# Kernel tuning notes

Measured on AMD Instinct MI355X. Metric: run time of the kernel, lower is better.

Reference implementation:

```python
import math
import jax, jax.numpy as jnp
import numpy as np

N_HEAD = 32
LAYER_NUMBER = 10  # cancels out: beta*alibi*L + alpha*QK^T*L = alibi + QK^T/sqrt(d)


def build_alibi(seq_len, n_head, dtype):
    # Faithful port of BLOOM's build_alibi_tensor -> [n_head, 1, seq_len]
    cp2 = 2 ** math.floor(math.log2(n_head))
    base = 2.0 ** (-(2.0 ** -(math.log2(cp2) - 3)))
    slopes = base ** np.arange(1, 1 + cp2)
    if cp2 != n_head:
        extra_base = 2.0 ** (-(2.0 ** -(math.log2(2 * cp2) - 3)))
        num_rem = min(cp2, n_head - cp2)
        slopes = np.concatenate([slopes, extra_base ** np.arange(1, 1 + 2 * num_rem, 2)])
    alibi = slopes[:, None, None] * np.arange(seq_len)[None, None, :]
    return jnp.asarray(alibi, dtype)


def setup_inputs() -> dict:
    key = jax.random.key(0)
    ks = jax.random.split(key, 6)
    B, S, H = 4, 1024, 4096
    return {
        "hidden_states": jax.random.normal(ks[0], (B, S, H), jnp.float32),
        "residual": jax.random.normal(ks[1], (B, S, H), jnp.float32),
        "qkv_w": jax.random.normal(ks[2], (3 * H, H), jnp.float32) * 0.02,
        "qkv_b": jnp.zeros((3 * H,), jnp.float32),
        "dense_w": jax.random.normal(ks[3], (H, H), jnp.float32) * 0.02,
        "dense_b": jnp.zeros((H,), jnp.float32),
    }


def reference(hidden_states, residual, qkv_w, qkv_b, dense_w, dense_b):
    B, S, H = hidden_states.shape
    nh = N_HEAD
    d = H // nh
    # fused qkv projection: [B,S,3H] -> [B,S,nh,3d] -> split
    mixed = (hidden_states @ qkv_w.T + qkv_b).reshape(B, S, nh, 3 * d)
    q, k, v = jnp.split(mixed, 3, axis=-1)  # each [B,S,nh,d]

    alibi = build_alibi(S, nh, hidden_states.dtype)  # [nh,1,S]
    # beta*alibi + alpha*QK^T, then *layer_number in scaled softmax == alibi + QK^T/sqrt(d)
    scores = jnp.einsum("bqhd,bkhd->bhqk", q, k) / math.sqrt(d) + alibi[None]  # [B,nh,S,S]

    causal = jnp.tril(jnp.ones((S, S), bool))  # [S,S], True = attend
    scores = jnp.where(causal, scores, jnp.asarray(-10000.0, scores.dtype))
    # softmax in fp32 (attention_softmax_in_fp32), then zero masked entries like *(~padded_causal_mask)
    probs = jax.nn.softmax(scores.astype(jnp.float32), axis=-1) * causal
    probs = probs.astype(v.dtype)

    ctx = jnp.einsum("bhqk,bkhd->bqhd", probs, v).reshape(B, S, H)
    out = ctx @ dense_w.T + dense_b + residual  # dropout_add with p=0 / eval
    return out
```

## Files before the change

kernel.cpp:

```cpp
#include <hip/hip_runtime.h>
#include <hip/hip_bf16.h>

typedef __attribute__((ext_vector_type(8))) short bf16x8;
typedef __attribute__((ext_vector_type(4))) short short4v;
typedef __attribute__((ext_vector_type(4))) float f32x4;

#define MFMA16(A, B, C) __builtin_amdgcn_mfma_f32_16x16x32_bf16((A), (B), (C), 0, 0, 0)
#define GLDS16(g, l)                                                            \
  __builtin_amdgcn_global_load_lds(                                             \
      (const __attribute__((address_space(1))) void*)(g),                       \
      (__attribute__((address_space(3))) void*)(l), 16, 0, 0)

__device__ __forceinline__ short f2bf(float f) {
  union { float f; unsigned u; } v; v.f = f;
  return (short)((v.u + 0x7fffu + ((v.u >> 16) & 1u)) >> 16);
}

__device__ __forceinline__ void blk_barrier() {
  asm volatile("" ::: "memory");
  __builtin_amdgcn_s_barrier();
  asm volatile("" ::: "memory");
}

__global__ __launch_bounds__(256) void cvt_kernel(const float* __restrict__ in,
                                                  short* __restrict__ out, int n4) {
  int i = blockIdx.x * 256 + threadIdx.x;
  const int stride = gridDim.x * 256;
  for (; i < n4; i += stride) {
    f32x4 v = ((const f32x4*)in)[i];
    short4v o;
    o[0] = f2bf(v[0]); o[1] = f2bf(v[1]); o[2] = f2bf(v[2]); o[3] = f2bf(v[3]);
    ((short4v*)out)[i] = o;
  }
}

__global__ __launch_bounds__(512, 2) void gemm_bt8(const short* __restrict__ A,
                                                   const short* __restrict__ B,
                                                   const float* __restrict__ bias,
                                                   const float* __restrict__ resid,
                                                   short* __restrict__ Cb,
                                                   float* __restrict__ Cf,
                                                   int Mtiles, int Nn, int K, int mode) {
  __shared__ short sA[2][2][8192];
  __shared__ short sB[2][2][8192];
  const int tid = threadIdx.x;
  const int w = tid >> 6, l = tid & 63;
  const int wm = w >> 2, wn = w & 3;
  const int fr = l & 15, g4 = l >> 4, sx = l & 7;

  const int nwg = gridDim.x;
  const int qq = nwg >> 3, rr = nwg & 7;
  const int xcd = blockIdx.x & 7, sub = blockIdx.x >> 3;
  const int swz = (xcd < rr ? xcd * (qq + 1) : rr * (qq + 1) + (xcd - rr) * qq) + sub;
  const int rowBase = (swz % Mtiles) * 256;
  const int colBase = (swz / Mtiles) * 256;

  const int NT = K >> 6;
  const int swcol = ((l & 7) ^ (l >> 3)) * 8;
  const short* Ag = A + (size_t)(rowBase + w * 8 + (l >> 3)) * K + swcol;
  const short* Bg = B + (size_t)(colBase + w * 8 + (l >> 3)) * K + swcol;
  const size_t q1 = (size_t)64 * K;
  const size_t hh = (size_t)128 * K;

#define STAGE_A(buf, h, ko)                                     \
  GLDS16(Ag + (h) * hh + (ko), &sA[buf][h][w * 512]);           \
  GLDS16(Ag + (h) * hh + q1 + (ko), &sA[buf][h][(8 + w) * 512]);
#define STAGE_B(buf, h, ko)                                     \
  GLDS16(Bg + (h) * hh + (ko), &sB[buf][h][w * 512]);           \
  GLDS16(Bg + (h) * hh + q1 + (ko), &sB[buf][h][(8 + w) * 512]);
#define RD_A(buf, m, ks) \
  (*(const bf16x8*)&sA[buf][wm][(((m) * 16 + fr) << 6) + ((((ks) * 4 + g4) ^ sx) << 3)])
#define RD_B(buf, nf, ks) \
  (*(const bf16x8*)&sB[buf][wn >> 1][((((wn & 1) * 64) + (nf) * 16 + fr) << 6) + ((((ks) * 4 + g4) ^ sx) << 3)])

  f32x4 acc[8][4];
#pragma unroll
  for (int m = 0; m < 8; m++)
#pragma unroll
    for (int n = 0; n < 4; n++) acc[m][n] = (f32x4)(0.0f);

  STAGE_A(0, 0, 0); STAGE_A(0, 1, 0);
  STAGE_B(0, 0, 0); STAGE_B(0, 1, 0);

  for (int t = 0; t < NT; ++t) {
    const int cur = t & 1, nxt = cur ^ 1;
    const size_t ko = (size_t)(t + 1) << 6;
    bf16x8 bfr[4][2], af[2][2];
    if (t + 1 < NT) {
      STAGE_A(nxt, 0, ko); STAGE_A(nxt, 1, ko);
      asm volatile("s_waitcnt vmcnt(4)" ::: "memory");
    } else {
      asm volatile("s_waitcnt vmcnt(0)" ::: "memory");
    }
    blk_barrier();
#pragma unroll
    for (int nf = 0; nf < 4; nf++) {
      bfr[nf][0] = RD_B(cur, nf, 0);
      bfr[nf][1] = RD_B(cur, nf, 1);
    }
    af[0][0] = RD_A(cur, 0, 0); af[0][1] = RD_A(cur, 0, 1);
    af[1][0] = RD_A(cur, 1, 0); af[1][1] = RD_A(cur, 1, 1);
    __builtin_amdgcn_s_setprio(1);
#pragma unroll
    for (int mi = 0; mi < 2; mi++)
#pragma unroll
      for (int nf = 0; nf < 4; nf++) {
        acc[mi][nf] = MFMA16(af[mi][0], bfr[nf][0], acc[mi][nf]);
        acc[mi][nf] = MFMA16(af[mi][1], bfr[nf][1], acc[mi][nf]);
      }
    __builtin_amdgcn_s_setprio(0);
    blk_barrier();
#pragma unroll
    for (int p = 1; p < 4; p++) {
      af[0][0] = RD_A(cur, 2 * p, 0);     af[0][1] = RD_A(cur, 2 * p, 1);
      af[1][0] = RD_A(cur, 2 * p + 1, 0); af[1][1] = RD_A(cur, 2 * p + 1, 1);
      if (p == 1 && t + 1 < NT) {
        STAGE_B(nxt, 0, ko); STAGE_B(nxt, 1, ko);
      }
      blk_barrier();
      __builtin_amdgcn_s_setprio(1);
#pragma unroll
      for (int mi = 0; mi < 2; mi++)
#pragma unroll
        for (int nf = 0; nf < 4; nf++) {
          acc[2 * p + mi][nf] = MFMA16(af[mi][0], bfr[nf][0], acc[2 * p + mi][nf]);
          acc[2 * p + mi][nf] = MFMA16(af[mi][1], bfr[nf][1], acc[2 * p + mi][nf]);
        }
      __builtin_amdgcn_s_setprio(0);
      blk_barrier();
    }
  }

#pragma unroll
  for (int m = 0; m < 8; m++) {
    const int row0 = rowBase + wm * 128 + m * 16 + g4 * 4;
#pragma unroll
    for (int n = 0; n < 4; n++) {
      const int col = colBase + wn * 64 + n * 16 + fr;
      const float bc = bias[col];
#pragma unroll
      for (int j = 0; j < 4; j++) {
        const size_t idx = (size_t)(row0 + j) * Nn + col;
        const float v = acc[m][n][j] + bc;
        if (mode == 0) Cb[idx] = f2bf(v);
        else Cf[idx] = v + resid[idx];
      }
    }
  }
#undef STAGE_A
#undef STAGE_B
#undef RD_A
#undef RD_B
}

__global__ __launch_bounds__(256) void vtrans_kernel(const short* __restrict__ mixed,
                                                     short* __restrict__ vt) {
  __shared__ short tl[64][132];
  const int tid = threadIdx.x;
  const int st = blockIdx.x;
  const int bh = blockIdx.y;
  const int b = bh >> 5, h = bh & 31;
  const short* src = mixed + (size_t)(b * 1024 + st * 64) * 12288 + h * 384 + 256;
#pragma unroll
  for (int it = 0; it < 8; it++) {
    int idx = (tid + it * 256) * 4;
    int row = idx >> 7, col = idx & 127;
    *(short4v*)&tl[row][col] = *(const short4v*)(src + row * 12288 + col);
  }
  __syncthreads();
  short* dst = vt + (size_t)bh * 128 * 1024 + st * 64;
#pragma unroll
  for (int it = 0; it < 8; it++) {
    int o = (tid + it * 256) * 4;
    int d = o >> 6, t4 = o & 63;
    short4v w;
    w[0] = tl[t4][d]; w[1] = tl[t4 + 1][d]; w[2] = tl[t4 + 2][d]; w[3] = tl[t4 + 3][d];
    *(short4v*)(dst + d * 1024 + t4) = w;
  }
}

__global__ __launch_bounds__(256, 2) void attn_kernel(const short* __restrict__ mixed,
                                                      const short* __restrict__ vt,
                                                      short* __restrict__ ctx) {
  __shared__ short sK[2][64 * 128];
  __shared__ short sV[2][128 * 64];
  __shared__ unsigned p_lds[4][16 * 36];
  const int tid = threadIdx.x;
  const int w = tid >> 6, l = tid & 63;
  const int g = l >> 4, f = l & 15, f7 = l & 7;

  const int bidx = blockIdx.x;
  const int xcd = bidx & 7, idx = bidx >> 3;
  const int bh = (xcd << 4) | (idx >> 4);
  const int qt = idx & 15;
  const int b = bh >> 5, h = bh & 31;
  const int qw = qt * 64 + w * 16;
  const float scale = 0.08838834764831845f;
  const float slope = exp2f(-0.25f * (float)(h + 1));

  const short* qptr = mixed + (size_t)b * 1024 * 12288 + h * 384;
  const short* kptr = qptr + 128;
  const short* vtp = vt + (size_t)bh * 128 * 1024;

  bf16x8 qf[4];
  {
    const short* qrow = qptr + (size_t)(qw + f) * 12288 + (g << 3);
#pragma unroll
    for (int ks = 0; ks < 4; ks++) qf[ks] = *(const bf16x8*)(qrow + ks * 32);
  }

#define STAGE_K(buf, kt)                                                        \
  {                                                                             \
    _Pragma("unroll") for (int c4 = 0; c4 < 4; c4++) {                          \
      const int c = c4 * 4 + w;                                                 \
      const int r = c * 4 + (l >> 4);                                           \
      GLDS16(kptr + (size_t)((kt) + r) * 12288 + (((l & 15) ^ (r & 7)) << 3),   \
             &sK[buf][c << 9]);                                                 \
    }                                                                           \
  }
#define STAGE_V(buf, kt)                                                        \
  {                                                                             \
    _Pragma("unroll") for (int c4 = 0; c4 < 4; c4++) {                          \
      const int c = c4 * 4 + w;                                                 \
      const int r = c * 8 + (l >> 3);                                           \
      GLDS16(vtp + (size_t)r * 1024 + (kt) + (((l & 7) ^ (r & 7)) << 3),        \
             &sV[buf][c << 9]);                                                 \
    }                                                                           \
  }

  f32x4 acc[8];
#pragma unroll
  for (int n = 0; n < 8; n++) acc[n] = (f32x4)(0.0f);
  float mrun = -1e30f, lrun = 0.0f;
  const int q = qw + f;
  unsigned* pw = p_lds[w];

  const int TT = qt + 1;
  STAGE_K(0, 0);
  STAGE_V(0, 0);

  for (int t = 0; t < TT; ++t) {
    const int cur = t & 1, nxt = cur ^ 1;
    const int kt = t << 6;
    if (t + 1 < TT) {
      STAGE_K(nxt, kt + 64);
      STAGE_V(nxt, kt + 64);
      asm volatile("s_waitcnt vmcnt(8)" ::: "memory");
    } else {
      asm volatile("s_waitcnt vmcnt(0)" ::: "memory");
    }
    blk_barrier();

    f32x4 s[4];
#pragma unroll
    for (int ksub = 0; ksub < 4; ksub++) {
      s[ksub] = (f32x4)(0.0f);
      const int r = ksub * 16 + f;
#pragma unroll
      for (int ks = 0; ks < 4; ks++) {
        bf16x8 kf = *(const bf16x8*)&sK[cur][(r << 7) + ((((ks << 2) + g) ^ f7) << 3)];
        s[ksub] = MFMA16(kf, qf[ks], s[ksub]);
      }
    }

    float ev[4][4];
    float tmax = -1e30f;
#pragma unroll
    for (int ksub = 0; ksub < 4; ksub++)
#pragma unroll
      for (int j = 0; j < 4; j++) {
        const int k = kt + ksub * 16 + g * 4 + j;
        float v = s[ksub][j] * scale + slope * (float)k;
        if (k > q) v = -1e30f;
        ev[ksub][j] = v;
        tmax = fmaxf(tmax, v);
      }
    tmax = fmaxf(tmax, __shfl_xor(tmax, 16));
    tmax = fmaxf(tmax, __shfl_xor(tmax, 32));
    const float mnew = fmaxf(mrun, tmax);
    const float asc = __expf(mrun - mnew);
    float psum = 0.0f;
    unsigned* pr = pw + f * 36;
#pragma unroll
    for (int ksub = 0; ksub < 4; ksub++) {
      float e0 = __expf(ev[ksub][0] - mnew);
      float e1 = __expf(ev[ksub][1] - mnew);
      float e2 = __expf(ev[ksub][2] - mnew);
      float e3 = __expf(ev[ksub][3] - mnew);
      psum += (e0 + e1) + (e2 + e3);
      unsigned w0 = (unsigned)(unsigned short)f2bf(e0) |
                    ((unsigned)(unsigned short)f2bf(e1) << 16);
      unsigned w1 = (unsigned)(unsigned short)f2bf(e2) |
                    ((unsigned)(unsigned short)f2bf(e3) << 16);
      pr[ksub * 8 + g * 2] = w0;
      pr[ksub * 8 + g * 2 + 1] = w1;
    }
    psum += __shfl_xor(psum, 16);
    psum += __shfl_xor(psum, 32);
    lrun = lrun * asc + psum;
    mrun = mnew;

    float ascB[4];
#pragma unroll
    for (int j = 0; j < 4; j++) ascB[j] = __shfl(asc, 20 * g + j);
#pragma unroll
    for (int n = 0; n < 8; n++)
#pragma unroll
      for (int j = 0; j < 4; j++) acc[n][j] *= ascB[j];

    bf16x8 pa0 = *(const bf16x8*)(pw + f * 36 + (g << 2));
    bf16x8 pa1 = *(const bf16x8*)(pw + f * 36 + 16 + (g << 2));
#pragma unroll
    for (int n = 0; n < 8; n++) {
      const int dr = (n << 4) + f;
      bf16x8 vf0 = *(const bf16x8*)&sV[cur][(dr << 6) + ((g ^ f7) << 3)];
      acc[n] = MFMA16(pa0, vf0, acc[n]);
      bf16x8 vf1 = *(const bf16x8*)&sV[cur][(dr << 6) + (((4 + g) ^ f7) << 3)];
      acc[n] = MFMA16(pa1, vf1, acc[n]);
    }
    blk_barrier();
  }

  const float linv = 1.0f / lrun;
  float invB[4];
#pragma unroll
  for (int j = 0; j < 4; j++) invB[j] = __shfl(linv, 20 * g + j);
  const int trow = b * 1024 + qw + (g << 2);
#pragma unroll
  for (int n = 0; n < 8; n++) {
    const int col = h * 128 + (n << 4) + f;
#pragma unroll
    for (int j = 0; j < 4; j++)
      ctx[(size_t)(trow + j) * 4096 + col] = f2bf(acc[n][j] * invB[j]);
  }
#undef STAGE_K
#undef STAGE_V
}

extern "C" void kernel_launch(void* const* d_in, const int* in_sizes, int n_in,
                              void* d_out, int out_size, void* d_ws, size_t ws_size,
                              hipStream_t stream) {
  const float* hs = (const float*)d_in[0];
  const float* resid = (const float*)d_in[1];
  const float* qkv_w = (const float*)d_in[2];
  const float* qkv_b = (const float*)d_in[3];
  const float* dense_w = (const float*)d_in[4];
  const float* dense_b = (const float*)d_in[5];
  float* out = (float*)d_out;

  short* hs_b = (short*)d_ws;
  short* wqkv_b = hs_b + (size_t)16777216;
  short* wd_b = wqkv_b + (size_t)50331648;
  short* mixed = wd_b + (size_t)16777216;
  short* vt = wqkv_b;
  short* ctx = hs_b;

  cvt_kernel<<<1024, 256, 0, stream>>>(hs, hs_b, 16777216 / 4);
  cvt_kernel<<<1024, 256, 0, stream>>>(qkv_w, wqkv_b, 50331648 / 4);
  cvt_kernel<<<1024, 256, 0, stream>>>(dense_w, wd_b, 16777216 / 4);
  gemm_bt8<<<dim3(48 * 16), 512, 0, stream>>>(hs_b, wqkv_b, qkv_b, nullptr,
                                              mixed, nullptr, 16, 12288, 4096, 0);
  vtrans_kernel<<<dim3(16, 128), 256, 0, stream>>>(mixed, vt);
  attn_kernel<<<2048, 256, 0, stream>>>(mixed, vt, ctx);
  gemm_bt8<<<dim3(16 * 16), 512, 0, stream>>>(ctx, wd_b, dense_b, resid,
                                              nullptr, out, 16, 4096, 4096, 1);
}
```

Before: 808.3 us.

## Use smaller-tile double-buffered GEMM for dense projection to fill more CUs

Adds a new bf16 GEMM kernel with 128x256 tiles, K-step 32, double-buffered LDS via global_load_lds, an XCD-aware block swizzle and launch bounds allowing four blocks per CU. The dense output projection now uses it with 512 workgroups instead of 256 large-tile ones. The goal is to better occupy the 256 CUs on a GEMM that otherwise launches only one wave of blocks. The cost is shallower pipelining and more barriers per K step, since each step covers only 32 elements of K.

```diff
diff --git a/kernel.cpp b/kernel.cpp
--- a/kernel.cpp
+++ b/kernel.cpp
@@ -153,6 +153,92 @@
 #undef RD_B
 }
 
+__global__ __launch_bounds__(512, 4) void gemm_bt(const short* __restrict__ A,
+                                                  const short* __restrict__ B,
+                                                  const float* __restrict__ bias,
+                                                  const float* __restrict__ resid,
+                                                  short* __restrict__ Cb,
+                                                  float* __restrict__ Cf,
+                                                  int Mtiles, int Nn, int K, int mode) {
+  __shared__ short sA[2][128 * 32];
+  __shared__ short sB[2][256 * 32];
+  const int tid = threadIdx.x;
+  const int w = tid >> 6, l = tid & 63;
+  const int wm = w >> 2, wn = w & 3;
+  const int fr = l & 15, g4 = l >> 4;
+  const int slotx = (g4 ^ ((fr >> 1) & 3)) << 3;
+
+  const int nwg = gridDim.x;
+  const int qq = nwg >> 3, rr = nwg & 7;
+  const int xcd = blockIdx.x & 7, sub = blockIdx.x >> 3;
+  const int swz = (xcd < rr ? xcd * (qq + 1) : rr * (qq + 1) + (xcd - rr) * qq) + sub;
+  const int rowBase = (swz % Mtiles) * 128;
+  const int colBase = (swz / Mtiles) * 256;
+
+  const int NT = K >> 5;
+  const int scol = ((l & 3) ^ ((l >> 3) & 3)) << 3;
+  const short* Ag = A + (size_t)(rowBase + w * 16 + (l >> 2)) * K + scol;
+  const short* Bg0 = B + (size_t)(colBase + w * 16 + (l >> 2)) * K + scol;
+  const short* Bg1 = Bg0 + (size_t)128 * K;
+
+  f32x4 acc[4][4];
+#pragma unroll
+  for (int m = 0; m < 4; m++)
+#pragma unroll
+    for (int n = 0; n < 4; n++) acc[m][n] = (f32x4)(0.0f);
+
+  GLDS16(Ag, &sA[0][w * 512]);
+  GLDS16(Bg0, &sB[0][w * 512]);
+  GLDS16(Bg1, &sB[0][(8 + w) * 512]);
+
+  for (int t = 0; t < NT; ++t) {
+    const int cur = t & 1, nxt = cur ^ 1;
+    const int ko = (t + 1) << 5;
+    if (t + 1 < NT) {
+      GLDS16(Ag + ko, &sA[nxt][w * 512]);
+      GLDS16(Bg0 + ko, &sB[nxt][w * 512]);
+      GLDS16(Bg1 + ko, &sB[nxt][(8 + w) * 512]);
+      asm volatile("s_waitcnt vmcnt(3)" ::: "memory");
+    } else {
+      asm volatile("s_waitcnt vmcnt(0)" ::: "memory");
+    }
+    blk_barrier();
+
+    bf16x8 af[4], bfr[4];
+#pragma unroll
+    for (int m = 0; m < 4; m++)
+      af[m] = *(const bf16x8*)&sA[cur][(wm * 64 + m * 16 + fr) * 32 + slotx];
+#pragma unroll
+    for (int nf = 0; nf < 4; nf++)
+      bfr[nf] = *(const bf16x8*)&sB[cur][(wn * 64 + nf * 16 + fr) * 32 + slotx];
+    __builtin_amdgcn_s_setprio(1);
+#pragma unroll
+    for (int m = 0; m < 4; m++)
+#pragma unroll
+      for (int nf = 0; nf < 4; nf++)
+        acc[m][nf] = MFMA16(af[m], bfr[nf], acc[m][nf]);
+    __builtin_amdgcn_s_setprio(0);
+    blk_barrier();
+  }
+
+#pragma unroll
+  for (int m = 0; m < 4; m++) {
+    const int row0 = rowBase + wm * 64 + m * 16 + g4 * 4;
+#pragma unroll
+    for (int n = 0; n < 4; n++) {
+      const int col = colBase + wn * 64 + n * 16 + fr;
+      const float bc = bias[col];
+#pragma unroll
+      for (int j = 0; j < 4; j++) {
+        const size_t idx = (size_t)(row0 + j) * Nn + col;
+        const float v = acc[m][n][j] + bc;
+        if (mode == 0) Cb[idx] = f2bf(v);
+        else Cf[idx] = v + resid[idx];
+      }
+    }
+  }
+}
+
 __global__ __launch_bounds__(256) void vtrans_kernel(const short* __restrict__ mixed,
                                                      short* __restrict__ vt) {
   __shared__ short tl[64][132];
@@ -362,6 +448,6 @@
                                               mixed, nullptr, 16, 12288, 4096, 0);
   vtrans_kernel<<<dim3(16, 128), 256, 0, stream>>>(mixed, vt);
   attn_kernel<<<2048, 256, 0, stream>>>(mixed, vt, ctx);
-  gemm_bt8<<<dim3(16 * 16), 512, 0, stream>>>(ctx, wd_b, dense_b, resid,
-                                              nullptr, out, 16, 4096, 4096, 1);
-}
+  gemm_bt<<<dim3(32 * 16), 512, 0, stream>>>(ctx, wd_b, dense_b, resid,
+                                             nullptr, out, 32, 4096, 4096, 1);
+}
```

Measured after the change: 791.1 us (median of 2 runs). 2.1% less time.
